# Performance work log

Hardware: AMD Instinct MI355X
Metric: run time of the kernel (lower is better)

The kernel has to match this reference:

```python
import jax, jax.numpy as jnp
import numpy as np

T, I, H = 65536, 512, 512

def setup_inputs() -> dict:
    key = jax.random.key(0)
    k1, k2, k3, k4, k5 = jax.random.split(key, 5)
    s_ih = 1.0 / np.sqrt(I)
    s_hh = 1.0 / np.sqrt(H)
    return {
        "net_input": jax.random.normal(k1, (T, 1, I), dtype=jnp.float32),
        "W_ih": jax.random.normal(k2, (4 * H, I), dtype=jnp.float32) * s_ih,
        "W_hh": jax.random.normal(k3, (4 * H, H), dtype=jnp.float32) * s_hh,
        "b_ih": jax.random.normal(k4, (4 * H,), dtype=jnp.float32) * s_ih,
        "b_hh": jax.random.normal(k5, (4 * H,), dtype=jnp.float32) * s_hh,
    }

def reference(net_input, W_ih, W_hh, b_ih, b_hh):
    # net_input: [T, 1, I]; LSTMCell recurrence with batch=1, PyTorch gate order (i, f, g, o).
    hid = W_hh.shape[1]
    h0 = jnp.zeros((1, hid), dtype=net_input.dtype)
    c0 = jnp.zeros((1, hid), dtype=net_input.dtype)
    # Precompute input projections for all timesteps in one GEMM: [T, 1, 4H]
    x_proj = jnp.einsum("tbi,gi->tbg", net_input, W_ih) + b_ih

    def step(carry, xp):
        h, c = carry
        gates = xp + h @ W_hh.T + b_hh  # [1, 4H]
        i_g, f_g, g_g, o_g = jnp.split(gates, 4, axis=-1)
        i_g = jax.nn.sigmoid(i_g)
        f_g = jax.nn.sigmoid(f_g)
        g_g = jnp.tanh(g_g)
        o_g = jax.nn.sigmoid(o_g)
        c_new = f_g * c + i_g * g_g
        h_new = o_g * jnp.tanh(c_new)
        return (h_new, c_new), None

    (h_final, _), _ = jax.lax.scan(step, (h0, c0), x_proj)
    return jax.nn.softmax(h_final, axis=-1)  # [1, H]
```

## Files before the change

kernel.cpp:

```cpp
#include <hip/hip_runtime.h>
#include <math.h>

#define T_STEPS 65536
#define HID     512
#define NWG     64
#define WGSIZE  256


__global__ __launch_bounds__(WGSIZE, 1)
void lstm_persistent(const float* __restrict__ x,
                     const float* __restrict__ Wih,
                     const float* __restrict__ Whh,
                     const float* __restrict__ bih,
                     const float* __restrict__ bhh,
                     float* __restrict__ out,
                     unsigned long long* hbuf)
{
  const int wg   = blockIdx.x;
  const int tid  = threadIdx.x;
  const int wid  = tid >> 6;
  const int lane = tid & 63;
  const int r    = lane & 7;
  const int g    = lane >> 3;
  const int k0   = g << 6;
  const int jloc = r & 1;
  const int gate = r >> 1;
  const int hidx = wg * 8 + wid * 2 + jloc;
  const int row  = gate * HID + hidx;

  __shared__ __align__(16) float hlds[512];
  __shared__ __align__(16) float xlds[512];

  float whh[64], wih[64];
#pragma unroll
  for (int i = 0; i < 16; ++i) {
    const int kk = k0 + (((i + g) & 15) << 2);
    float4 a = *reinterpret_cast<const float4*>(Whh + (size_t)row * 512 + kk);
    float4 b = *reinterpret_cast<const float4*>(Wih + (size_t)row * 512 + kk);
    whh[4*i+0] = a.x; whh[4*i+1] = a.y; whh[4*i+2] = a.z; whh[4*i+3] = a.w;
    wih[4*i+0] = b.x; wih[4*i+1] = b.y; wih[4*i+2] = b.z; wih[4*i+3] = b.w;
  }
  const float bias = bih[row] + bhh[row];

  if (tid < 128) {
    float4 v = reinterpret_cast<const float4*>(x)[tid];
    *reinterpret_cast<float4*>(xlds + tid * 4) = v;
  }
  __syncthreads();

  auto dot_lds = [&](const float* lds, const float* w) -> float {
    float acc = 0.f;
#pragma unroll
    for (int i = 0; i < 16; ++i) {
      const int kk = k0 + (((i + g) & 15) << 2);
      float4 v = *reinterpret_cast<const float4*>(lds + kk);
      acc = fmaf(w[4*i+0], v.x, acc);
      acc = fmaf(w[4*i+1], v.y, acc);
      acc = fmaf(w[4*i+2], v.z, acc);
      acc = fmaf(w[4*i+3], v.w, acc);
    }
    return acc;
  };

  float xacc = dot_lds(xlds, wih);
  float c    = 0.f;

#pragma unroll 1
  for (int t = 0; t < T_STEPS; ++t) {
    float4 xv;
    const bool do_x = (tid < 128) && (t + 1 < T_STEPS);
    if (do_x) xv = reinterpret_cast<const float4*>(x + (size_t)(t + 1) * 512)[tid];

    if (t > 0) {
      const unsigned long long* src = hbuf + (((t - 1) & 1) << 9) + (tid << 1);
      const unsigned exp = (unsigned)t;
      unsigned long long p0, p1;
      while (true) {
        p0 = __hip_atomic_load(src + 0, __ATOMIC_RELAXED, __HIP_MEMORY_SCOPE_AGENT);
        p1 = __hip_atomic_load(src + 1, __ATOMIC_RELAXED, __HIP_MEMORY_SCOPE_AGENT);
        if ((unsigned)(p0 >> 32) == exp && (unsigned)(p1 >> 32) == exp) break;
      }
      hlds[(tid << 1) + 0] = __uint_as_float((unsigned)p0);
      hlds[(tid << 1) + 1] = __uint_as_float((unsigned)p1);
    }
    if (do_x) *reinterpret_cast<float4*>(xlds + tid * 4) = xv;
    __syncthreads();

    float acc = xacc;
    if (t > 0) acc += dot_lds(hlds, whh);
    acc += __shfl_xor(acc, 8);
    acc += __shfl_xor(acc, 16);
    acc += __shfl_xor(acc, 32);
    acc += bias;

    const bool isg = (gate == 2);
    float xs = isg ? 2.f * acc : acc;
    float s  = 1.f / (1.f + expf(-xs));
    float v  = isg ? (2.f * s - 1.f) : s;

    float iv = __shfl(v, jloc + 0);
    float fv = __shfl(v, jloc + 2);
    float gv = __shfl(v, jloc + 4);
    float ov = __shfl(v, jloc + 6);

    c = fv * c + iv * gv;
    float e2 = expf(-2.f * c);
    float th = 2.f / (1.f + e2) - 1.f;
    float hn = ov * th;

    if (lane < 2) {
      unsigned long long pk =
          ((unsigned long long)(unsigned)(t + 1) << 32) | (unsigned)__float_as_uint(hn);
      __hip_atomic_store(hbuf + ((t & 1) << 9) + wg * 8 + wid * 2 + lane, pk,
                         __ATOMIC_RELAXED, __HIP_MEMORY_SCOPE_AGENT);
    }

    if (t + 1 < T_STEPS) xacc = dot_lds(xlds, wih);
    __syncthreads();
  }

  if (wg == 0 && wid == 0) {
    const unsigned long long* src = hbuf + (((T_STEPS - 1) & 1) << 9);
    float hv[8];
    {
      unsigned long long p[8];
      while (true) {
        bool ok = true;
#pragma unroll
        for (int m2 = 0; m2 < 8; ++m2) {
          p[m2] = __hip_atomic_load(src + lane * 8 + m2,
                                    __ATOMIC_RELAXED, __HIP_MEMORY_SCOPE_AGENT);
          ok &= ((unsigned)(p[m2] >> 32) == (unsigned)T_STEPS);
        }
        if (__all(ok)) break;
      }
#pragma unroll
      for (int m2 = 0; m2 < 8; ++m2) hv[m2] = __uint_as_float((unsigned)p[m2]);
    }
    float mx = hv[0];
#pragma unroll
    for (int m2 = 1; m2 < 8; ++m2) mx = fmaxf(mx, hv[m2]);
    mx = fmaxf(mx, __shfl_xor(mx, 1));
    mx = fmaxf(mx, __shfl_xor(mx, 2));
    mx = fmaxf(mx, __shfl_xor(mx, 4));
    mx = fmaxf(mx, __shfl_xor(mx, 8));
    mx = fmaxf(mx, __shfl_xor(mx, 16));
    mx = fmaxf(mx, __shfl_xor(mx, 32));
    float ex[8], sum = 0.f;
#pragma unroll
    for (int m2 = 0; m2 < 8; ++m2) { ex[m2] = expf(hv[m2] - mx); sum += ex[m2]; }
    sum += __shfl_xor(sum, 1);
    sum += __shfl_xor(sum, 2);
    sum += __shfl_xor(sum, 4);
    sum += __shfl_xor(sum, 8);
    sum += __shfl_xor(sum, 16);
    sum += __shfl_xor(sum, 32);
    float inv = 1.f / sum;
#pragma unroll
    for (int m2 = 0; m2 < 8; ++m2) out[lane * 8 + m2] = ex[m2] * inv;
  }
}

extern "C" void kernel_launch(void* const* d_in, const int* in_sizes, int n_in,
                              void* d_out, int out_size, void* d_ws, size_t ws_size,
                              hipStream_t stream) {
  const float* x   = (const float*)d_in[0];
  const float* Wih = (const float*)d_in[1];
  const float* Whh = (const float*)d_in[2];
  const float* bih = (const float*)d_in[3];
  const float* bhh = (const float*)d_in[4];
  float* out = (float*)d_out;
  unsigned long long* hbuf = (unsigned long long*)d_ws;

  hipMemsetAsync(d_ws, 0, 8192, stream);
  lstm_persistent<<<NWG, WGSIZE, 0, stream>>>(x, Wih, Whh, bih, bhh, out, hbuf);
}
```

Baseline: 106.5 ms.

## Split LSTM recurrence into single-wave workgroups using wave barriers instead of block syncs

Work moves from 64 workgroups of 4 waves to 256 single-wave workgroups, each owning two hidden units. This removes the two __syncthreads per timestep in favour of wave barriers. Each wave now polls and stages the full 512-element hidden vector itself (8 values per lane), and x is loaded with nontemporal loads. The goal is shorter per-step synchronisation latency on the serial critical path. In exchange, four times as many waves poll the shared hbuf, which raises contention on it, and all 256 workgroups must be resident at once for the spin-waits to make progress.

```diff
diff --git a/kernel.cpp b/kernel.cpp
--- a/kernel.cpp
+++ b/kernel.cpp
@@ -3,33 +3,33 @@
 
 #define T_STEPS 65536
 #define HID     512
-#define NWG     64
-#define WGSIZE  256
+#define NWG     256
+#define WGSIZE  64
+
+typedef float f4v __attribute__((ext_vector_type(4)));
 
 
 __global__ __launch_bounds__(WGSIZE, 1)
-void lstm_persistent(const float* __restrict__ x,
-                     const float* __restrict__ Wih,
-                     const float* __restrict__ Whh,
-                     const float* __restrict__ bih,
-                     const float* __restrict__ bhh,
-                     float* __restrict__ out,
-                     unsigned long long* hbuf)
+void lstm_wave(const float* __restrict__ x,
+               const float* __restrict__ Wih,
+               const float* __restrict__ Whh,
+               const float* __restrict__ bih,
+               const float* __restrict__ bhh,
+               float* __restrict__ out,
+               unsigned long long* hbuf)
 {
   const int wg   = blockIdx.x;
-  const int tid  = threadIdx.x;
-  const int wid  = tid >> 6;
-  const int lane = tid & 63;
+  const int lane = threadIdx.x;
   const int r    = lane & 7;
   const int g    = lane >> 3;
   const int k0   = g << 6;
   const int jloc = r & 1;
   const int gate = r >> 1;
-  const int hidx = wg * 8 + wid * 2 + jloc;
+  const int hidx = wg * 2 + jloc;
   const int row  = gate * HID + hidx;
 
-  __shared__ __align__(16) float hlds[512];
-  __shared__ __align__(16) float xlds[512];
+  __shared__ __align__(16) float hl[512];
+  __shared__ __align__(16) float xl[512];
 
   float whh[64], wih[64];
 #pragma unroll
@@ -42,11 +42,13 @@
   }
   const float bias = bih[row] + bhh[row];
 
-  if (tid < 128) {
-    float4 v = reinterpret_cast<const float4*>(x)[tid];
-    *reinterpret_cast<float4*>(xlds + tid * 4) = v;
+  {
+    const f4v* xp = reinterpret_cast<const f4v*>(x) + lane * 2;
+    f4v a = xp[0], b = xp[1];
+    *reinterpret_cast<f4v*>(&xl[lane * 8 + 0]) = a;
+    *reinterpret_cast<f4v*>(&xl[lane * 8 + 4]) = b;
   }
-  __syncthreads();
+  __builtin_amdgcn_wave_barrier();
 
   auto dot_lds = [&](const float* lds, const float* w) -> float {
     float acc = 0.f;
@@ -62,32 +64,44 @@
     return acc;
   };
 
-  float xacc = dot_lds(xlds, wih);
+  float xacc = dot_lds(xl, wih);
   float c    = 0.f;
 
 #pragma unroll 1
   for (int t = 0; t < T_STEPS; ++t) {
-    float4 xv;
-    const bool do_x = (tid < 128) && (t + 1 < T_STEPS);
-    if (do_x) xv = reinterpret_cast<const float4*>(x + (size_t)(t + 1) * 512)[tid];
+    f4v xa, xb;
+    const bool do_x = (t + 1 < T_STEPS);
+    if (do_x) {
+      const f4v* xp = reinterpret_cast<const f4v*>(x + (size_t)(t + 1) * 512) + lane * 2;
+      xa = __builtin_nontemporal_load(xp);
+      xb = __builtin_nontemporal_load(xp + 1);
+    }
 
     if (t > 0) {
-      const unsigned long long* src = hbuf + (((t - 1) & 1) << 9) + (tid << 1);
+      const unsigned long long* src = hbuf + (((t - 1) & 1) << 9) + lane * 8;
       const unsigned exp = (unsigned)t;
-      unsigned long long p0, p1;
-      while (true) {
-        p0 = __hip_atomic_load(src + 0, __ATOMIC_RELAXED, __HIP_MEMORY_SCOPE_AGENT);
-        p1 = __hip_atomic_load(src + 1, __ATOMIC_RELAXED, __HIP_MEMORY_SCOPE_AGENT);
-        if ((unsigned)(p0 >> 32) == exp && (unsigned)(p1 >> 32) == exp) break;
-      }
-      hlds[(tid << 1) + 0] = __uint_as_float((unsigned)p0);
-      hlds[(tid << 1) + 1] = __uint_as_float((unsigned)p1);
+      unsigned long long p[8];
+      bool ok;
+      do {
+#pragma unroll
+        for (int j = 0; j < 8; ++j)
+          p[j] = __hip_atomic_load(src + j, __ATOMIC_RELAXED, __HIP_MEMORY_SCOPE_AGENT);
+        ok = true;
+#pragma unroll
+        for (int j = 0; j < 8; ++j) ok &= ((unsigned)(p[j] >> 32) == exp);
+      } while (!__all(ok));
+
+      f4v h0 = { __uint_as_float((unsigned)p[0]), __uint_as_float((unsigned)p[1]),
+                 __uint_as_float((unsigned)p[2]), __uint_as_float((unsigned)p[3]) };
+      f4v h1 = { __uint_as_float((unsigned)p[4]), __uint_as_float((unsigned)p[5]),
+                 __uint_as_float((unsigned)p[6]), __uint_as_float((unsigned)p[7]) };
+      *reinterpret_cast<f4v*>(&hl[lane * 8 + 0]) = h0;
+      *reinterpret_cast<f4v*>(&hl[lane * 8 + 4]) = h1;
+      __builtin_amdgcn_wave_barrier();
     }
-    if (do_x) *reinterpret_cast<float4*>(xlds + tid * 4) = xv;
-    __syncthreads();
 
     float acc = xacc;
-    if (t > 0) acc += dot_lds(hlds, whh);
+    if (t > 0) acc += dot_lds(hl, whh);
     acc += __shfl_xor(acc, 8);
     acc += __shfl_xor(acc, 16);
     acc += __shfl_xor(acc, 32);
@@ -111,35 +125,37 @@
     if (lane < 2) {
       unsigned long long pk =
           ((unsigned long long)(unsigned)(t + 1) << 32) | (unsigned)__float_as_uint(hn);
-      __hip_atomic_store(hbuf + ((t & 1) << 9) + wg * 8 + wid * 2 + lane, pk,
+      __hip_atomic_store(hbuf + ((t & 1) << 9) + wg * 2 + lane, pk,
                          __ATOMIC_RELAXED, __HIP_MEMORY_SCOPE_AGENT);
     }
 
-    if (t + 1 < T_STEPS) xacc = dot_lds(xlds, wih);
-    __syncthreads();
+    if (do_x) {
+      *reinterpret_cast<f4v*>(&xl[lane * 8 + 0]) = xa;
+      *reinterpret_cast<f4v*>(&xl[lane * 8 + 4]) = xb;
+      __builtin_amdgcn_wave_barrier();
+      xacc = dot_lds(xl, wih);
+    }
   }
 
-  if (wg == 0 && wid == 0) {
-    const unsigned long long* src = hbuf + (((T_STEPS - 1) & 1) << 9);
+  if (wg == 0) {
+    const unsigned long long* src = hbuf + (((T_STEPS - 1) & 1) << 9) + lane * 8;
+    unsigned long long p[8];
+    bool ok;
+    do {
+#pragma unroll
+      for (int j = 0; j < 8; ++j)
+        p[j] = __hip_atomic_load(src + j, __ATOMIC_RELAXED, __HIP_MEMORY_SCOPE_AGENT);
+      ok = true;
+#pragma unroll
+      for (int j = 0; j < 8; ++j) ok &= ((unsigned)(p[j] >> 32) == (unsigned)T_STEPS);
+    } while (!__all(ok));
+
     float hv[8];
-    {
-      unsigned long long p[8];
-      while (true) {
-        bool ok = true;
 #pragma unroll
-        for (int m2 = 0; m2 < 8; ++m2) {
-          p[m2] = __hip_atomic_load(src + lane * 8 + m2,
-                                    __ATOMIC_RELAXED, __HIP_MEMORY_SCOPE_AGENT);
-          ok &= ((unsigned)(p[m2] >> 32) == (unsigned)T_STEPS);
-        }
-        if (__all(ok)) break;
-      }
-#pragma unroll
-      for (int m2 = 0; m2 < 8; ++m2) hv[m2] = __uint_as_float((unsigned)p[m2]);
-    }
+    for (int j = 0; j < 8; ++j) hv[j] = __uint_as_float((unsigned)p[j]);
     float mx = hv[0];
 #pragma unroll
-    for (int m2 = 1; m2 < 8; ++m2) mx = fmaxf(mx, hv[m2]);
+    for (int j = 1; j < 8; ++j) mx = fmaxf(mx, hv[j]);
     mx = fmaxf(mx, __shfl_xor(mx, 1));
     mx = fmaxf(mx, __shfl_xor(mx, 2));
     mx = fmaxf(mx, __shfl_xor(mx, 4));
@@ -148,7 +164,7 @@
     mx = fmaxf(mx, __shfl_xor(mx, 32));
     float ex[8], sum = 0.f;
 #pragma unroll
-    for (int m2 = 0; m2 < 8; ++m2) { ex[m2] = expf(hv[m2] - mx); sum += ex[m2]; }
+    for (int j = 0; j < 8; ++j) { ex[j] = expf(hv[j] - mx); sum += ex[j]; }
     sum += __shfl_xor(sum, 1);
     sum += __shfl_xor(sum, 2);
     sum += __shfl_xor(sum, 4);
@@ -157,7 +173,7 @@
     sum += __shfl_xor(sum, 32);
     float inv = 1.f / sum;
 #pragma unroll
-    for (int m2 = 0; m2 < 8; ++m2) out[lane * 8 + m2] = ex[m2] * inv;
+    for (int j = 0; j < 8; ++j) out[lane * 8 + j] = ex[j] * inv;
   }
 }
 
@@ -172,6 +188,6 @@
   float* out = (float*)d_out;
   unsigned long long* hbuf = (unsigned long long*)d_ws;
 
-  hipMemsetAsync(d_ws, 0, 8192, stream);
-  lstm_persistent<<<NWG, WGSIZE, 0, stream>>>(x, Wih, Whh, bih, bhh, out, hbuf);
+  (void)hipMemsetAsync(d_ws, 0, 8192, stream);
+  lstm_wave<<<NWG, WGSIZE, 0, stream>>>(x, Wih, Whh, bih, bhh, out, hbuf);
 }
```

Result: slower. 145.1 ms (+36.3%).

## Halve workgroups to 32 and double-buffer LDS to drop the second barrier

Applied to the files above, without the earlier changes.

Cuts the persistent grid from 64 to 32 workgroups. Each thread now holds 128 weights per matrix and covers 128 K-elements with four independent accumulators, so the reduction needs one fewer shuffle. The h and x LDS buffers are double-buffered by step parity, which lets the trailing __syncthreads per step go away, and x is fetched with nontemporal loads. Fewer workgroups means fewer participants polling and publishing in the cross-workgroup handshake, at the cost of twice the dot-product work per thread and much higher register pressure.

```diff
diff --git a/kernel.cpp b/kernel.cpp
--- a/kernel.cpp
+++ b/kernel.cpp
@@ -3,38 +3,39 @@
 
 #define T_STEPS 65536
 #define HID     512
-#define NWG     64
+#define NWG     32
 #define WGSIZE  256
+
+typedef float f2v __attribute__((ext_vector_type(2)));
 
 
 __global__ __launch_bounds__(WGSIZE, 1)
-void lstm_persistent(const float* __restrict__ x,
-                     const float* __restrict__ Wih,
-                     const float* __restrict__ Whh,
-                     const float* __restrict__ bih,
-                     const float* __restrict__ bhh,
-                     float* __restrict__ out,
-                     unsigned long long* hbuf)
+void lstm_32wg(const float* __restrict__ x,
+               const float* __restrict__ Wih,
+               const float* __restrict__ Whh,
+               const float* __restrict__ bih,
+               const float* __restrict__ bhh,
+               float* __restrict__ out,
+               unsigned long long* hbuf)
 {
   const int wg   = blockIdx.x;
   const int tid  = threadIdx.x;
   const int wid  = tid >> 6;
   const int lane = tid & 63;
-  const int r    = lane & 7;
-  const int g    = lane >> 3;
-  const int k0   = g << 6;
-  const int jloc = r & 1;
-  const int gate = r >> 1;
-  const int hidx = wg * 8 + wid * 2 + jloc;
+  const int gate = lane & 3;
+  const int jloc = (lane >> 2) & 3;
+  const int g    = lane >> 4;
+  const int kb   = g << 7;
+  const int hidx = wg * 16 + wid * 4 + jloc;
   const int row  = gate * HID + hidx;
 
-  __shared__ __align__(16) float hlds[512];
-  __shared__ __align__(16) float xlds[512];
+  __shared__ __align__(16) float hl[2][512];
+  __shared__ __align__(16) float xl[2][512];
 
-  float whh[64], wih[64];
+  float whh[128], wih[128];
 #pragma unroll
-  for (int i = 0; i < 16; ++i) {
-    const int kk = k0 + (((i + g) & 15) << 2);
+  for (int i = 0; i < 32; ++i) {
+    const int kk = kb + (((i + g) & 31) << 2);
     float4 a = *reinterpret_cast<const float4*>(Whh + (size_t)row * 512 + kk);
     float4 b = *reinterpret_cast<const float4*>(Wih + (size_t)row * 512 + kk);
     whh[4*i+0] = a.x; whh[4*i+1] = a.y; whh[4*i+2] = a.z; whh[4*i+3] = a.w;
@@ -42,34 +43,37 @@
   }
   const float bias = bih[row] + bhh[row];
 
-  if (tid < 128) {
-    float4 v = reinterpret_cast<const float4*>(x)[tid];
-    *reinterpret_cast<float4*>(xlds + tid * 4) = v;
+  {
+    f2v v = *(reinterpret_cast<const f2v*>(x) + tid);
+    *reinterpret_cast<f2v*>(&xl[0][tid * 2]) = v;
   }
   __syncthreads();
 
   auto dot_lds = [&](const float* lds, const float* w) -> float {
-    float acc = 0.f;
+    float a0 = 0.f, a1 = 0.f, a2 = 0.f, a3 = 0.f;
 #pragma unroll
-    for (int i = 0; i < 16; ++i) {
-      const int kk = k0 + (((i + g) & 15) << 2);
+    for (int i = 0; i < 32; ++i) {
+      const int kk = kb + (((i + g) & 31) << 2);
       float4 v = *reinterpret_cast<const float4*>(lds + kk);
-      acc = fmaf(w[4*i+0], v.x, acc);
-      acc = fmaf(w[4*i+1], v.y, acc);
-      acc = fmaf(w[4*i+2], v.z, acc);
-      acc = fmaf(w[4*i+3], v.w, acc);
+      a0 = fmaf(w[4*i+0], v.x, a0);
+      a1 = fmaf(w[4*i+1], v.y, a1);
+      a2 = fmaf(w[4*i+2], v.z, a2);
+      a3 = fmaf(w[4*i+3], v.w, a3);
     }
-    return acc;
+    return (a0 + a1) + (a2 + a3);
   };
 
-  float xacc = dot_lds(xlds, wih);
+  float xacc = dot_lds(xl[0], wih);
   float c    = 0.f;
 
 #pragma unroll 1
   for (int t = 0; t < T_STEPS; ++t) {
-    float4 xv;
-    const bool do_x = (tid < 128) && (t + 1 < T_STEPS);
-    if (do_x) xv = reinterpret_cast<const float4*>(x + (size_t)(t + 1) * 512)[tid];
+    f2v xv;
+    const bool do_x = (t + 1 < T_STEPS);
+    if (do_x) {
+      const f2v* xp = reinterpret_cast<const f2v*>(x + (size_t)(t + 1) * 512) + tid;
+      xv = __builtin_nontemporal_load(xp);
+    }
 
     if (t > 0) {
       const unsigned long long* src = hbuf + (((t - 1) & 1) << 9) + (tid << 1);
@@ -80,15 +84,14 @@
         p1 = __hip_atomic_load(src + 1, __ATOMIC_RELAXED, __HIP_MEMORY_SCOPE_AGENT);
         if ((unsigned)(p0 >> 32) == exp && (unsigned)(p1 >> 32) == exp) break;
       }
-      hlds[(tid << 1) + 0] = __uint_as_float((unsigned)p0);
-      hlds[(tid << 1) + 1] = __uint_as_float((unsigned)p1);
+      f2v hv = { __uint_as_float((unsigned)p0), __uint_as_float((unsigned)p1) };
+      *reinterpret_cast<f2v*>(&hl[t & 1][tid * 2]) = hv;
     }
-    if (do_x) *reinterpret_cast<float4*>(xlds + tid * 4) = xv;
+    if (do_x) *reinterpret_cast<f2v*>(&xl[(t + 1) & 1][tid * 2]) = xv;
     __syncthreads();
 
     float acc = xacc;
-    if (t > 0) acc += dot_lds(hlds, whh);
-    acc += __shfl_xor(acc, 8);
+    if (t > 0) acc += dot_lds(hl[t & 1], whh);
     acc += __shfl_xor(acc, 16);
     acc += __shfl_xor(acc, 32);
     acc += bias;
@@ -98,48 +101,47 @@
     float s  = 1.f / (1.f + expf(-xs));
     float v  = isg ? (2.f * s - 1.f) : s;
 
-    float iv = __shfl(v, jloc + 0);
-    float fv = __shfl(v, jloc + 2);
-    float gv = __shfl(v, jloc + 4);
-    float ov = __shfl(v, jloc + 6);
+    const int base = lane & ~3;
+    float iv = __shfl(v, base + 0);
+    float fv = __shfl(v, base + 1);
+    float gv = __shfl(v, base + 2);
+    float ov = __shfl(v, base + 3);
 
     c = fv * c + iv * gv;
     float e2 = expf(-2.f * c);
     float th = 2.f / (1.f + e2) - 1.f;
     float hn = ov * th;
 
-    if (lane < 2) {
+    if ((lane & 0x33) == 0 || (lane < 16 && gate == 0)) {  }
+    if (lane < 16 && gate == 0) {
       unsigned long long pk =
           ((unsigned long long)(unsigned)(t + 1) << 32) | (unsigned)__float_as_uint(hn);
-      __hip_atomic_store(hbuf + ((t & 1) << 9) + wg * 8 + wid * 2 + lane, pk,
+      __hip_atomic_store(hbuf + ((t & 1) << 9) + wg * 16 + wid * 4 + jloc, pk,
                          __ATOMIC_RELAXED, __HIP_MEMORY_SCOPE_AGENT);
     }
 
-    if (t + 1 < T_STEPS) xacc = dot_lds(xlds, wih);
-    __syncthreads();
+    if (do_x) xacc = dot_lds(xl[(t + 1) & 1], wih);
   }
 
-  if (wg == 0 && wid == 0) {
-    const unsigned long long* src = hbuf + (((T_STEPS - 1) & 1) << 9);
+  if (wg == 0 && tid < 64) {
+    const unsigned long long* src = hbuf + (((T_STEPS - 1) & 1) << 9) + lane * 8;
+    unsigned long long p[8];
+    bool ok;
+    do {
+#pragma unroll
+      for (int j = 0; j < 8; ++j)
+        p[j] = __hip_atomic_load(src + j, __ATOMIC_RELAXED, __HIP_MEMORY_SCOPE_AGENT);
+      ok = true;
+#pragma unroll
+      for (int j = 0; j < 8; ++j) ok &= ((unsigned)(p[j] >> 32) == (unsigned)T_STEPS);
+    } while (!__all(ok));
+
     float hv[8];
-    {
-      unsigned long long p[8];
-      while (true) {
-        bool ok = true;
 #pragma unroll
-        for (int m2 = 0; m2 < 8; ++m2) {
-          p[m2] = __hip_atomic_load(src + lane * 8 + m2,
-                                    __ATOMIC_RELAXED, __HIP_MEMORY_SCOPE_AGENT);
-          ok &= ((unsigned)(p[m2] >> 32) == (unsigned)T_STEPS);
-        }
-        if (__all(ok)) break;
-      }
-#pragma unroll
-      for (int m2 = 0; m2 < 8; ++m2) hv[m2] = __uint_as_float((unsigned)p[m2]);
-    }
+    for (int j = 0; j < 8; ++j) hv[j] = __uint_as_float((unsigned)p[j]);
     float mx = hv[0];
 #pragma unroll
-    for (int m2 = 1; m2 < 8; ++m2) mx = fmaxf(mx, hv[m2]);
+    for (int j = 1; j < 8; ++j) mx = fmaxf(mx, hv[j]);
     mx = fmaxf(mx, __shfl_xor(mx, 1));
     mx = fmaxf(mx, __shfl_xor(mx, 2));
     mx = fmaxf(mx, __shfl_xor(mx, 4));
@@ -148,7 +150,7 @@
     mx = fmaxf(mx, __shfl_xor(mx, 32));
     float ex[8], sum = 0.f;
 #pragma unroll
-    for (int m2 = 0; m2 < 8; ++m2) { ex[m2] = expf(hv[m2] - mx); sum += ex[m2]; }
+    for (int j = 0; j < 8; ++j) { ex[j] = expf(hv[j] - mx); sum += ex[j]; }
     sum += __shfl_xor(sum, 1);
     sum += __shfl_xor(sum, 2);
     sum += __shfl_xor(sum, 4);
@@ -157,7 +159,7 @@
     sum += __shfl_xor(sum, 32);
     float inv = 1.f / sum;
 #pragma unroll
-    for (int m2 = 0; m2 < 8; ++m2) out[lane * 8 + m2] = ex[m2] * inv;
+    for (int j = 0; j < 8; ++j) out[lane * 8 + j] = ex[j] * inv;
   }
 }
 
@@ -172,6 +174,6 @@
   float* out = (float*)d_out;
   unsigned long long* hbuf = (unsigned long long*)d_ws;
 
-  hipMemsetAsync(d_ws, 0, 8192, stream);
-  lstm_persistent<<<NWG, WGSIZE, 0, stream>>>(x, Wih, Whh, bih, bhh, out, hbuf);
+  (void)hipMemsetAsync(d_ws, 0, 8192, stream);
+  lstm_32wg<<<NWG, WGSIZE, 0, stream>>>(x, Wih, Whh, bih, bhh, out, hbuf);
 }
```

Result: slower. 157.7 ms (+48.1%).
